# Kernel optimization log

Hardware: AMD Instinct MI355X
Metric: run time of the kernel (lower is better)

## Reference

```python
import jax, jax.numpy as jnp
import numpy as np

N_ROIS, ROI_DIM, D, H, L, FF, NCLS = 200, 199, 192, 6, 3, 576, 2
EPS = 1e-5

def _ln(x, g, b):
    m = jnp.mean(x, axis=-1, keepdims=True)
    v = jnp.mean((x - m) ** 2, axis=-1, keepdims=True)
    return (x - m) * jax.lax.rsqrt(v + EPS) * g + b

def _gelu(x):
    return jax.nn.gelu(x, approximate=False)

def _mha(q, k, v, Wqkv, bqkv, Wo, bo):
    # q: [B,Q,D], k/v: [B,S,D]; Wqkv: [3,D,D], bqkv: [3,D]
    B, Q, _ = q.shape
    S = k.shape[1]
    Dh = D // H
    qp = (q @ Wqkv[0] + bqkv[0]).reshape(B, Q, H, Dh)
    kp = (k @ Wqkv[1] + bqkv[1]).reshape(B, S, H, Dh)
    vp = (v @ Wqkv[2] + bqkv[2]).reshape(B, S, H, Dh)
    scores = jnp.einsum('bqhd,bkhd->bhqk', qp, kp) / jnp.sqrt(jnp.float32(Dh))
    attn = jax.nn.softmax(scores, axis=-1)
    out = jnp.einsum('bhqk,bkhd->bqhd', attn, vp).reshape(B, Q, D)
    return out @ Wo + bo

def setup_inputs() -> dict:
    key = jax.random.key(0)
    ks = iter(jax.random.split(key, 40))
    r = lambda *s: jax.random.normal(next(ks), s, dtype=jnp.float32) * 0.02
    inp = {
        'x': jax.random.normal(next(ks), (256, N_ROIS * ROI_DIM), dtype=jnp.float32),
        # 200 distinct per-ROI tokenizers, stacked for a single batched GEMM
        'roi_W': r(N_ROIS, ROI_DIM, D), 'roi_b': r(N_ROIS, D),
        'roi_ln_g': jnp.ones((N_ROIS, D), jnp.float32), 'roi_ln_b': jnp.zeros((N_ROIS, D), jnp.float32),
        'pos_emb': r(N_ROIS, D),
        # encoder layers stacked on leading L dim
        'enc_Wqkv': r(L, 3, D, D), 'enc_bqkv': r(L, 3, D),
        'enc_Wo': r(L, D, D), 'enc_bo': r(L, D),
        'enc_ln1_g': jnp.ones((L, D), jnp.float32), 'enc_ln1_b': jnp.zeros((L, D), jnp.float32),
        'enc_W1': r(L, D, FF), 'enc_b1': r(L, FF),
        'enc_W2': r(L, FF, D), 'enc_b2': r(L, D),
        'enc_ln2_g': jnp.ones((L, D), jnp.float32), 'enc_ln2_b': jnp.zeros((L, D), jnp.float32),
        # attention pooling MHA
        'pool_Wqkv': r(3, D, D), 'pool_bqkv': r(3, D),
        'pool_Wo': r(D, D), 'pool_bo': r(D),
        # classifier head
        'cls_ln_g': jnp.ones((D,), jnp.float32), 'cls_ln_b': jnp.zeros((D,), jnp.float32),
        'cls_W1': r(D, D // 2), 'cls_b1': r(D // 2),
        'cls_W2': r(D // 2, D // 4), 'cls_b2': r(D // 4),
        'cls_W3': r(D // 4, NCLS), 'cls_b3': r(NCLS),
    }
    return inp

def reference(x, roi_W, roi_b, roi_ln_g, roi_ln_b, pos_emb,
              enc_Wqkv, enc_bqkv, enc_Wo, enc_bo, enc_ln1_g, enc_ln1_b,
              enc_W1, enc_b1, enc_W2, enc_b2, enc_ln2_g, enc_ln2_b,
              pool_Wqkv, pool_bqkv, pool_Wo, pool_bo,
              cls_ln_g, cls_ln_b, cls_W1, cls_b1, cls_W2, cls_b2, cls_W3, cls_b3):
    B = x.shape[0]
    roi = x.reshape(B, N_ROIS, ROI_DIM)
    # fused per-ROI Linear (200 distinct weights) as one batched GEMM
    tok = jnp.einsum('brf,rfd->brd', roi, roi_W) + roi_b  # [B,200,192]
    tok = _gelu(_ln(tok, roi_ln_g, roi_ln_b))  # dropout = identity (eval)
    tok = tok + pos_emb[None]
    # post-norm transformer encoder (PyTorch default norm_first=False)
    h = tok
    for i in range(L):
        a = _mha(h, h, h, enc_Wqkv[i], enc_bqkv[i], enc_Wo[i], enc_bo[i])
        h = _ln(h + a, enc_ln1_g[i], enc_ln1_b[i])
        f = _gelu(h @ enc_W1[i] + enc_b1[i]) @ enc_W2[i] + enc_b2[i]
        h = _ln(h + f, enc_ln2_g[i], enc_ln2_b[i])
    # MHA pooling: query = mean over ROI tokens
    q = jnp.mean(h, axis=1, keepdims=True)  # [B,1,D]
    pooled = _mha(q, h, h, pool_Wqkv, pool_bqkv, pool_Wo, pool_bo)[:, 0]  # [B,D]
    # classifier
    z = _ln(pooled, cls_ln_g, cls_ln_b)
    z = _gelu(z @ cls_W1 + cls_b1)
    z = _gelu(z @ cls_W2 + cls_b2)
    return z @ cls_W3 + cls_b3
```

## Files before the change

kernel.cpp:

```cpp
#include <hip/hip_runtime.h>
#include <math.h>


typedef unsigned short u16;
typedef unsigned int u32;
typedef __attribute__((ext_vector_type(8))) __bf16 bf16x8;
typedef __attribute__((ext_vector_type(4))) float f32x4;

#define GLL16(gp, lp) __builtin_amdgcn_global_load_lds(                 \
    (const __attribute__((address_space(1))) void*)(gp),                \
    (__attribute__((address_space(3))) void*)(lp), 16, 0, 0)

#define FENCE_VM()   do { asm volatile("s_waitcnt vmcnt(0)" ::: "memory");  \
                          __builtin_amdgcn_sched_barrier(0); } while (0)
#define FENCE_LGKM() do { asm volatile("s_waitcnt lgkmcnt(0)" ::: "memory");\
                          __builtin_amdgcn_sched_barrier(0); } while (0)

__device__ __forceinline__ u16 f2bf(float x) {
    u32 u = __float_as_uint(x);
    u = (u + 0x7FFFu + ((u >> 16) & 1u)) >> 16;
    return (u16)u;
}
__device__ __forceinline__ float bf2f(u16 h) {
    return __uint_as_float(((u32)h) << 16);
}

__device__ __forceinline__ float gelu_exact(float x) {
    return 0.5f * x * (1.0f + erff(x * 0.7071067811865475f));
}

__device__ __forceinline__ float wave_sum(float v) {
#pragma unroll
    for (int o = 32; o > 0; o >>= 1) v += __shfl_xor(v, o, 64);
    return v;
}
__device__ __forceinline__ float wave_max(float v) {
#pragma unroll
    for (int o = 32; o > 0; o >>= 1) v = fmaxf(v, __shfl_xor(v, o, 64));
    return v;
}
__device__ __forceinline__ float row_sum16(float v) {
    v += __shfl_xor(v, 1, 64); v += __shfl_xor(v, 2, 64);
    v += __shfl_xor(v, 4, 64); v += __shfl_xor(v, 8, 64);
    return v;
}

__device__ __forceinline__ f32x4 mfma_bf16(bf16x8 a, bf16x8 b, f32x4 c) {
    return __builtin_amdgcn_mfma_f32_16x16x32_bf16(a, b, c, 0, 0, 0);
}

__global__ void conv_wt(const float* __restrict__ W, u16* __restrict__ oh,
                        int K, int N)
{
    const long z = blockIdx.z;
    const int idx = blockIdx.x * 256 + threadIdx.x;
    if (idx >= K * N) return;
    const int k = idx / N, n = idx - k * N;
    const float x = W[z * K * N + idx];
    oh[z * (long)K * N + (long)n * K + k] = f2bf(x);
}

__global__ void conv_x(const float* __restrict__ x, u16* __restrict__ xh)
{
    const long idx = (long)blockIdx.x * 256 + threadIdx.x;
    if (idx >= 200L * 256 * 224) return;
    const int k = (int)(idx % 224);
    const long t = idx / 224;
    const int m = (int)(t % 256);
    const int z = (int)(t / 256);
    const float v = (k < 199) ? x[(long)m * 39800 + z * 199 + k] : 0.f;
    xh[idx] = f2bf(v);
}

__global__ void conv_roiw(const float* __restrict__ W, u16* __restrict__ oh)
{
    __shared__ float tile[32][33];
    const int z = blockIdx.z;
    const int k0 = blockIdx.x * 32;
    const int n0 = blockIdx.y * 32;
    for (int i = threadIdx.y; i < 32; i += 8) {
        const int k = k0 + i, n = n0 + threadIdx.x;
        tile[i][threadIdx.x] = (k < 199) ? W[((long)z * 199 + k) * 192 + n] : 0.f;
    }
    __syncthreads();
    for (int i = threadIdx.y; i < 32; i += 8) {
        const int n = n0 + i, k = k0 + threadIdx.x;
        const float v = tile[threadIdx.x][i];
        oh[((long)z * 192 + n) * 224 + k] = f2bf(v);
    }
}

template<int EPI>
__global__ __launch_bounds__(256, 3) void gemm_ns(
    const u16* __restrict__ Ah,
    const u16* __restrict__ Bh,
    const float* __restrict__ bias,
    float* __restrict__ C, u16* __restrict__ Ch,
    int N, int K)
{
    __shared__ u16 Ash[128][32];
    __shared__ u16 Bsh[192][32];

    const int tid = threadIdx.x;
    const int wave = tid >> 6, lane = tid & 63;
    const int lm = lane & 15, quad = lane >> 4;
    const int wm = wave >> 1, wn = wave & 1;
    const long m0 = (long)blockIdx.x * 128;
    const int n0 = blockIdx.y * 192;
    const int lrow = lane >> 2;
    const int lch  = (((lane & 3) ^ (lrow & 3)) * 8);
    const int sq   = (quad ^ (lm & 3)) * 8;

    const u16* pA0h = Ah + (m0 + wave * 32 +  0 + lrow) * K + lch;
    const u16* pA1h = Ah + (m0 + wave * 32 + 16 + lrow) * K + lch;
    const u16* pB0h = Bh + (long)(n0 + wave * 48 +  0 + lrow) * K + lch;
    const u16* pB1h = Bh + (long)(n0 + wave * 48 + 16 + lrow) * K + lch;
    const u16* pB2h = Bh + (long)(n0 + wave * 48 + 32 + lrow) * K + lch;

    auto stage = [&](int k0) {
        GLL16(pA0h + k0, &Ash[wave * 32][0]);
        GLL16(pA1h + k0, &Ash[wave * 32 + 16][0]);
        GLL16(pB0h + k0, &Bsh[wave * 48][0]);
        GLL16(pB1h + k0, &Bsh[wave * 48 + 16][0]);
        GLL16(pB2h + k0, &Bsh[wave * 48 + 32][0]);
    };

    f32x4 acc[4][6];
#pragma unroll
    for (int i = 0; i < 4; i++)
#pragma unroll
        for (int j = 0; j < 6; j++)
#pragma unroll
            for (int r = 0; r < 4; r++) acc[i][j][r] = 0.f;

    const int kt = K >> 5;
    stage(0);
    FENCE_VM();
    __syncthreads();

    for (int t = 0; t < kt; t++) {
        bf16x8 afh[4];
#pragma unroll
        for (int mi = 0; mi < 4; mi++)
            afh[mi] = *(const bf16x8*)&Ash[wm * 64 + mi * 16 + lm][sq];
#pragma unroll
        for (int jh = 0; jh < 2; jh++) {
            bf16x8 bfh[3];
#pragma unroll
            for (int j = 0; j < 3; j++)
                bfh[j] = *(const bf16x8*)&Bsh[wn * 96 + (jh * 3 + j) * 16 + lm][sq];
#pragma unroll
            for (int mi = 0; mi < 4; mi++)
#pragma unroll
                for (int j = 0; j < 3; j++)
                    acc[mi][jh * 3 + j] =
                        mfma_bf16(afh[mi], bfh[j], acc[mi][jh * 3 + j]);
        }
        if (t + 1 < kt) {
            __syncthreads();
            stage((t + 1) << 5);
            FENCE_VM();
            __syncthreads();
        }
    }

#pragma unroll
    for (int mi = 0; mi < 4; mi++) {
        const long rowb = m0 + wm * 64 + mi * 16 + quad * 4;
#pragma unroll
        for (int nj = 0; nj < 6; nj++) {
            const int col = n0 + wn * 96 + nj * 16 + lm;
            const float bv = bias[col];
#pragma unroll
            for (int r = 0; r < 4; r++) {
                float v = acc[mi][nj][r] + bv;
                if (EPI == 0) {
                    C[(rowb + r) * N + col] = v;
                } else {
                    if (EPI == 2) v = gelu_exact(v);
                    Ch[(rowb + r) * N + col] = f2bf(v);
                }
            }
        }
    }
}

__global__ __launch_bounds__(256, 3) void gemm_ln(
    const u16* __restrict__ Ah,
    const u16* __restrict__ Bh,
    const float* __restrict__ bias,
    u16* __restrict__ Hh, u16* __restrict__ Hl,
    const float* __restrict__ lng, const float* __restrict__ lnb,
    int K)
{
    __shared__ u16 Ash[128][32];
    __shared__ u16 Bsh[192][32];

    const int tid = threadIdx.x;
    const int wave = tid >> 6, lane = tid & 63;
    const int lm = lane & 15, quad = lane >> 4;
    const long m0 = (long)blockIdx.x * 128;
    const int lrow = lane >> 2;
    const int lch  = (((lane & 3) ^ (lrow & 3)) * 8);
    const int sq   = (quad ^ (lm & 3)) * 8;

    const u16* pA0h = Ah + (m0 + wave * 32 +  0 + lrow) * K + lch;
    const u16* pA1h = Ah + (m0 + wave * 32 + 16 + lrow) * K + lch;
    const u16* pB0h = Bh + (long)(wave * 48 +  0 + lrow) * K + lch;
    const u16* pB1h = Bh + (long)(wave * 48 + 16 + lrow) * K + lch;
    const u16* pB2h = Bh + (long)(wave * 48 + 32 + lrow) * K + lch;

    auto stage = [&](int k0) {
        GLL16(pA0h + k0, &Ash[wave * 32][0]);
        GLL16(pA1h + k0, &Ash[wave * 32 + 16][0]);
        GLL16(pB0h + k0, &Bsh[wave * 48][0]);
        GLL16(pB1h + k0, &Bsh[wave * 48 + 16][0]);
        GLL16(pB2h + k0, &Bsh[wave * 48 + 32][0]);
    };

    f32x4 acc[2][12];
#pragma unroll
    for (int i = 0; i < 2; i++)
#pragma unroll
        for (int j = 0; j < 12; j++)
#pragma unroll
            for (int r = 0; r < 4; r++) acc[i][j][r] = 0.f;

    const int kt = K >> 5;
    stage(0);
    FENCE_VM();
    __syncthreads();

    for (int t = 0; t < kt; t++) {
        bf16x8 afh[2];
#pragma unroll
        for (int mi = 0; mi < 2; mi++)
            afh[mi] = *(const bf16x8*)&Ash[wave * 32 + mi * 16 + lm][sq];
#pragma unroll
        for (int g = 0; g < 4; g++) {
            bf16x8 bfh[3];
#pragma unroll
            for (int j = 0; j < 3; j++)
                bfh[j] = *(const bf16x8*)&Bsh[g * 48 + j * 16 + lm][sq];
#pragma unroll
            for (int mi = 0; mi < 2; mi++)
#pragma unroll
                for (int j = 0; j < 3; j++) {
                    const int ni = g * 3 + j;
                    acc[mi][ni] = mfma_bf16(afh[mi], bfh[j], acc[mi][ni]);
                }
        }
        if (t + 1 < kt) {
            __syncthreads();
            stage((t + 1) << 5);
            FENCE_VM();
            __syncthreads();
        }
    }

    float gv[12], bv2[12], biasv[12];
#pragma unroll
    for (int ni = 0; ni < 12; ni++) {
        const int col = ni * 16 + lm;
        gv[ni] = lng[col]; bv2[ni] = lnb[col]; biasv[ni] = bias[col];
    }
#pragma unroll
    for (int mi = 0; mi < 2; mi++) {
#pragma unroll
        for (int r = 0; r < 4; r++) {
            const long row = m0 + wave * 32 + mi * 16 + quad * 4 + r;
            const long rb = row * 192;
            float vals[12];
            float s = 0.f;
#pragma unroll
            for (int ni = 0; ni < 12; ni++) {
                const int col = ni * 16 + lm;
                const float hval = bf2f(Hh[rb + col]) + bf2f(Hl[rb + col]);
                vals[ni] = acc[mi][ni][r] + biasv[ni] + hval;
                s += vals[ni];
            }
            const float mean = row_sum16(s) * (1.f / 192.f);
            float ss = 0.f;
#pragma unroll
            for (int ni = 0; ni < 12; ni++) {
                vals[ni] -= mean;
                ss += vals[ni] * vals[ni];
            }
            const float var = row_sum16(ss) * (1.f / 192.f);
            const float rsr = 1.f / sqrtf(var + 1e-5f);
#pragma unroll
            for (int ni = 0; ni < 12; ni++) {
                const int col = ni * 16 + lm;
                const float y = vals[ni] * rsr * gv[ni] + bv2[ni];
                const u16 hb = f2bf(y);
                Hh[rb + col] = hb;
                Hl[rb + col] = f2bf(y - bf2f(hb));
            }
        }
    }
}

__global__ __launch_bounds__(256, 3) void tok_mfma(
    const u16* __restrict__ xh,
    const u16* __restrict__ wth,
    const float* __restrict__ roi_b,
    const float* __restrict__ lng, const float* __restrict__ lnb,
    const float* __restrict__ pos,
    u16* __restrict__ hh, u16* __restrict__ hl)
{
    __shared__ u16 Ash[128][32];
    __shared__ u16 Bsh[192][32];

    const int tid = threadIdx.x;
    const int wave = tid >> 6, lane = tid & 63;
    const int lm = lane & 15, quad = lane >> 4;
    const int m0 = blockIdx.x * 128;
    const int z = blockIdx.y;
    const int lrow = lane >> 2;
    const int lch  = (((lane & 3) ^ (lrow & 3)) * 8);
    const int sq   = (quad ^ (lm & 3)) * 8;
    const int K = 224;

    const u16* pA0h = xh + ((long)z * 256 + m0 + wave * 32 +  0 + lrow) * K + lch;
    const u16* pA1h = xh + ((long)z * 256 + m0 + wave * 32 + 16 + lrow) * K + lch;
    const u16* pB0h = wth + ((long)z * 192 + wave * 48 +  0 + lrow) * K + lch;
    const u16* pB1h = wth + ((long)z * 192 + wave * 48 + 16 + lrow) * K + lch;
    const u16* pB2h = wth + ((long)z * 192 + wave * 48 + 32 + lrow) * K + lch;

    auto stage = [&](int k0) {
        GLL16(pA0h + k0, &Ash[wave * 32][0]);
        GLL16(pA1h + k0, &Ash[wave * 32 + 16][0]);
        GLL16(pB0h + k0, &Bsh[wave * 48][0]);
        GLL16(pB1h + k0, &Bsh[wave * 48 + 16][0]);
        GLL16(pB2h + k0, &Bsh[wave * 48 + 32][0]);
    };

    f32x4 acc[2][12];
#pragma unroll
    for (int i = 0; i < 2; i++)
#pragma unroll
        for (int j = 0; j < 12; j++)
#pragma unroll
            for (int r = 0; r < 4; r++) acc[i][j][r] = 0.f;

    stage(0);
    FENCE_VM();
    __syncthreads();
    for (int t = 0; t < 7; t++) {
        bf16x8 afh[2];
#pragma unroll
        for (int mi = 0; mi < 2; mi++)
            afh[mi] = *(const bf16x8*)&Ash[wave * 32 + mi * 16 + lm][sq];
#pragma unroll
        for (int g = 0; g < 4; g++) {
            bf16x8 bfh[3];
#pragma unroll
            for (int j = 0; j < 3; j++)
                bfh[j] = *(const bf16x8*)&Bsh[g * 48 + j * 16 + lm][sq];
#pragma unroll
            for (int mi = 0; mi < 2; mi++)
#pragma unroll
                for (int j = 0; j < 3; j++) {
                    const int ni = g * 3 + j;
                    acc[mi][ni] = mfma_bf16(afh[mi], bfh[j], acc[mi][ni]);
                }
        }
        if (t + 1 < 7) {
            __syncthreads();
            stage((t + 1) << 5);
            FENCE_VM();
            __syncthreads();
        }
    }

    float gv[12], bv2[12], biasv[12], pv[12];
#pragma unroll
    for (int ni = 0; ni < 12; ni++) {
        const int col = ni * 16 + lm;
        gv[ni]    = lng[z * 192 + col];
        bv2[ni]   = lnb[z * 192 + col];
        biasv[ni] = roi_b[z * 192 + col];
        pv[ni]    = pos[z * 192 + col];
    }
#pragma unroll
    for (int mi = 0; mi < 2; mi++) {
#pragma unroll
        for (int r = 0; r < 4; r++) {
            const int brow = m0 + wave * 32 + mi * 16 + quad * 4 + r;
            float vals[12];
            float s = 0.f;
#pragma unroll
            for (int ni = 0; ni < 12; ni++) {
                vals[ni] = acc[mi][ni][r] + biasv[ni];
                s += vals[ni];
            }
            const float mean = row_sum16(s) * (1.f / 192.f);
            float ss = 0.f;
#pragma unroll
            for (int ni = 0; ni < 12; ni++) {
                vals[ni] -= mean;
                ss += vals[ni] * vals[ni];
            }
            const float var = row_sum16(ss) * (1.f / 192.f);
            const float rsr = 1.f / sqrtf(var + 1e-5f);
            const long ob = ((long)brow * 200 + z) * 192;
#pragma unroll
            for (int ni = 0; ni < 12; ni++) {
                const int col = ni * 16 + lm;
                const float y = gelu_exact(vals[ni] * rsr * gv[ni] + bv2[ni]) + pv[ni];
                const u16 hb = f2bf(y);
                hh[ob + col] = hb;
                hl[ob + col] = f2bf(y - bf2f(hb));
            }
        }
    }
}

template<int EPI>
__global__ __launch_bounds__(256) void gemm_kernel(
    const float* __restrict__ A, int lda, long strideA,
    const float* __restrict__ Bw, long strideB,
    const float* __restrict__ bias, long strideBias,
    float* __restrict__ C, int ldc, long strideC,
    int M, int N, int K, int ldb)
{
    __shared__ float As[16][132];
    __shared__ float Bs[16][68];

    const int z = blockIdx.z;
    const float* Ab    = A    + (long)z * strideA;
    const float* Bb    = Bw   + (long)z * strideB;
    const float* biasb = bias + (long)z * strideBias;
    float*       Cb    = C    + (long)z * strideC;

    const int row0 = blockIdx.x * 128;
    const int col0 = blockIdx.y * 64;
    const int tid  = threadIdx.x;
    const int tm = tid >> 4;
    const int tn = tid & 15;

    const int la_m = tid >> 1;
    const int la_k = (tid & 1) * 8;
    const int lb_k = tid >> 4;
    const int lb_n = (tid & 15) * 4;

    const float* bcol = Bb + (col0 + lb_n);
    const float* arow = Ab + (long)(row0 + la_m) * lda;
    const bool vecA = ((lda & 3) == 0) &&
                      ((((unsigned long long)(const void*)arow) & 15ull) == 0ull);

    float acc[8][4];
#pragma unroll
    for (int i = 0; i < 8; i++)
#pragma unroll
        for (int j = 0; j < 4; j++) acc[i][j] = 0.f;

    for (int k0 = 0; k0 < K; k0 += 16) {
        if (vecA && (k0 + 16 <= K)) {
            float4 v0 = *(const float4*)(arow + k0 + la_k);
            float4 v1 = *(const float4*)(arow + k0 + la_k + 4);
            As[la_k + 0][la_m] = v0.x; As[la_k + 1][la_m] = v0.y;
            As[la_k + 2][la_m] = v0.z; As[la_k + 3][la_m] = v0.w;
            As[la_k + 4][la_m] = v1.x; As[la_k + 5][la_m] = v1.y;
            As[la_k + 6][la_m] = v1.z; As[la_k + 7][la_m] = v1.w;
        } else {
#pragma unroll
            for (int i = 0; i < 8; i++) {
                int k = k0 + la_k + i;
                As[la_k + i][la_m] = (k < K) ? arow[k] : 0.f;
            }
        }
        {
            int k = k0 + lb_k;
            float4 v = make_float4(0.f, 0.f, 0.f, 0.f);
            if (k < K) v = *(const float4*)(bcol + (long)k * ldb);
            *(float4*)&Bs[lb_k][lb_n] = v;
        }
        __syncthreads();
#pragma unroll
        for (int kk = 0; kk < 16; kk++) {
            float4 a0 = *(const float4*)&As[kk][tm * 8];
            float4 a1 = *(const float4*)&As[kk][tm * 8 + 4];
            float4 b4 = *(const float4*)&Bs[kk][tn * 4];
            float av[8] = {a0.x, a0.y, a0.z, a0.w, a1.x, a1.y, a1.z, a1.w};
            float bv[4] = {b4.x, b4.y, b4.z, b4.w};
#pragma unroll
            for (int i = 0; i < 8; i++)
#pragma unroll
                for (int j = 0; j < 4; j++) acc[i][j] += av[i] * bv[j];
        }
        __syncthreads();
    }

    const int gcol = col0 + tn * 4;
    float4 bv4 = *(const float4*)(biasb + gcol);
#pragma unroll
    for (int i = 0; i < 8; i++) {
        int grow = row0 + tm * 8 + i;
        float4 o;
        o.x = acc[i][0] + bv4.x; o.y = acc[i][1] + bv4.y;
        o.z = acc[i][2] + bv4.z; o.w = acc[i][3] + bv4.w;
        if (EPI == 1) {
            o.x = gelu_exact(o.x); o.y = gelu_exact(o.y);
            o.z = gelu_exact(o.z); o.w = gelu_exact(o.w);
        }
        *(float4*)(Cb + (long)grow * ldc + gcol) = o;
    }
}

__global__ __launch_bounds__(256, 2) void attn_enc_mfma(
    const u16* __restrict__ qkvh, u16* __restrict__ outh)
{
    __shared__ u16 Ksh[208][40];
    __shared__ u16 Vth[32][224];
    __shared__ u16 Pbuf[4][2][16][40];

    const int bh = blockIdx.x;
    const int b = bh / 6, h = bh % 6;
    const int tid = threadIdx.x;
    const int wave = tid >> 6, lane = tid & 63;
    const int lm = lane & 15, quad = lane >> 4;
    const int nq = (wave == 0) ? 4 : 3;

    uint4 qh[4];
#pragma unroll
    for (int i = 0; i < 4; i++) {
        if (i < nq) {
            int qt = wave + 4 * i;
            int qrow = qt * 16 + lm; if (qrow > 199) qrow = 199;
            const long off = (long)(b * 200 + qrow) * 576 + h * 32 + quad * 8;
            qh[i] = *(const uint4*)(qkvh + off);
        }
    }

    if (wave < 2) {
        const int sub = wave * 64 + lane;
#pragma unroll
        for (int rep = 0; rep < 7; rep++) {
            const int idx = rep * 128 + sub;
            if (idx < 208 * 4) {
                const int key = idx >> 2, ch = idx & 3;
                const bool valid = key < 200;
                const long roff = (long)(b * 200 + (valid ? key : 0)) * 576
                                  + h * 32 + 192 + ch * 8;
                uint4 v = valid ? *(const uint4*)(qkvh + roff)
                                : make_uint4(0, 0, 0, 0);
                *(uint4*)(&Ksh[0][0] + key * 40 + ch * 8) = v;
            }
        }
    } else {
        const int sub = (wave - 2) * 64 + lane;
#pragma unroll
        for (int rep = 0; rep < 4; rep++) {
            const int idx = rep * 128 + sub;
            if (idx < 224 * 2) {
                const int key = idx >> 1, hf = idx & 1;
                const bool valid = key < 200;
                const long roff = (long)(b * 200 + (valid ? key : 0)) * 576
                                  + h * 32 + 384 + hf * 16;
                uint4 v0 = valid ? *(const uint4*)(qkvh + roff)
                                 : make_uint4(0, 0, 0, 0);
                uint4 v1 = valid ? *(const uint4*)(qkvh + roff + 8)
                                 : make_uint4(0, 0, 0, 0);
                const u16* p0 = (const u16*)&v0;
                const u16* p1 = (const u16*)&v1;
#pragma unroll
                for (int j = 0; j < 8; j++) {
                    Vth[hf * 16 + j][key]     = p0[j];
                    Vth[hf * 16 + 8 + j][key] = p1[j];
                }
            }
        }
    }
    __syncthreads();

    const float scale = 0.17677669529663688f;
    int par = 0;
    float lrow[4][4];
    f32x4 accO[4][2];

#pragma unroll
    for (int i = 0; i < 4; i++) {
        if (i >= nq) continue;
        const bf16x8 qhf = *(const bf16x8*)&qh[i];
        float s[13][4];
#pragma unroll
        for (int ni = 0; ni < 13; ni++) {
            bf16x8 kh8 = *(const bf16x8*)&Ksh[ni * 16 + lm][quad * 8];
            f32x4 c = {0.f, 0.f, 0.f, 0.f};
            c = mfma_bf16(qhf, kh8, c);
            const bool masked = (ni * 16 + lm) >= 200;
#pragma unroll
            for (int r = 0; r < 4; r++)
                s[ni][r] = masked ? -1e30f : c[r] * scale;
        }
#pragma unroll
        for (int r = 0; r < 4; r++) {
            float pm = s[0][r];
#pragma unroll
            for (int ni = 1; ni < 13; ni++) pm = fmaxf(pm, s[ni][r]);
            pm = fmaxf(pm, __shfl_xor(pm, 1, 64));
            pm = fmaxf(pm, __shfl_xor(pm, 2, 64));
            pm = fmaxf(pm, __shfl_xor(pm, 4, 64));
            pm = fmaxf(pm, __shfl_xor(pm, 8, 64));
            float ps = 0.f;
#pragma unroll
            for (int ni = 0; ni < 13; ni++) {
                float e = __expf(s[ni][r] - pm);
                s[ni][r] = e;
                ps += e;
            }
            ps += __shfl_xor(ps, 1, 64);
            ps += __shfl_xor(ps, 2, 64);
            ps += __shfl_xor(ps, 4, 64);
            ps += __shfl_xor(ps, 8, 64);
            lrow[i][r] = ps;
            accO[i][0][r] = 0.f;
            accO[i][1][r] = 0.f;
        }
#pragma unroll
        for (int ck = 0; ck < 7; ck++) {
            const int pb = par & 1; par++;
#pragma unroll
            for (int tl = 0; tl < 2; tl++) {
                const int t = 2 * ck + tl;
#pragma unroll
                for (int r = 0; r < 4; r++) {
                    const float val = (t < 13) ? s[t][r] : 0.f;
                    Pbuf[wave][pb][quad * 4 + r][tl * 16 + lm] = f2bf(val);
                }
            }
            FENCE_LGKM();
            const bf16x8 pa = *(const bf16x8*)&Pbuf[wave][pb][lm][quad * 8];
#pragma unroll
            for (int nt = 0; nt < 2; nt++) {
                bf16x8 vh8 = *(const bf16x8*)&Vth[nt * 16 + lm][ck * 32 + quad * 8];
                accO[i][nt] = mfma_bf16(pa, vh8, accO[i][nt]);
            }
        }
    }

#pragma unroll
    for (int i = 0; i < 4; i++) {
        if (i >= nq) continue;
        const int qt = wave + 4 * i;
#pragma unroll
        for (int r = 0; r < 4; r++) {
            const int qrow = qt * 16 + quad * 4 + r;
            if (qrow >= 200) continue;
            const float inv = 1.f / lrow[i][r];
            const long ob = (long)(b * 200 + qrow) * 192 + h * 32 + lm;
            outh[ob]      = f2bf(accO[i][0][r] * inv);
            outh[ob + 16] = f2bf(accO[i][1][r] * inv);
        }
    }
}

__global__ __launch_bounds__(192) void mean_tokens_pair(
    const u16* __restrict__ hh, const u16* __restrict__ hl, float* __restrict__ qmean)
{
    const int b = blockIdx.x, d = threadIdx.x;
    float s = 0.f;
    for (int r = 0; r < 200; r++) {
        const long idx = ((long)b * 200 + r) * 192 + d;
        s += bf2f(hh[idx]) + bf2f(hl[idx]);
    }
    qmean[b * 192 + d] = s * (1.f / 200.f);
}

__global__ __launch_bounds__(64) void attn_pool(
    const float* __restrict__ qp, const float* __restrict__ kv,
    float* __restrict__ out)
{
    __shared__ float p[200];
    const int b = blockIdx.x / 6, h = blockIdx.x % 6;
    const int lane = threadIdx.x;

    const float* qrow = qp + b * 192 + h * 32;
    float qr[32];
#pragma unroll
    for (int u = 0; u < 8; u++) {
        float4 t = *(const float4*)(qrow + 4 * u);
        qr[4 * u] = t.x; qr[4 * u + 1] = t.y;
        qr[4 * u + 2] = t.z; qr[4 * u + 3] = t.w;
    }
    const float scale = 0.17677669529663688f;
    const float* kb = kv + (long)(b * 200) * 384 + h * 32;
    float s[4];
    float mymax = -1e30f;
#pragma unroll
    for (int g = 0; g < 4; g++) {
        int j = lane + 64 * g;
        if (j < 200) {
            const float* kr = kb + (long)j * 384;
            float acc = 0.f;
#pragma unroll
            for (int u = 0; u < 8; u++) {
                float4 k4 = *(const float4*)(kr + 4 * u);
                acc += qr[4 * u] * k4.x + qr[4 * u + 1] * k4.y +
                       qr[4 * u + 2] * k4.z + qr[4 * u + 3] * k4.w;
            }
            s[g] = acc * scale;
            mymax = fmaxf(mymax, s[g]);
        } else {
            s[g] = -1e30f;
        }
    }
    float mx = wave_max(mymax);
    float psum = 0.f;
#pragma unroll
    for (int g = 0; g < 4; g++) {
        int j = lane + 64 * g;
        if (j < 200) {
            float e = __expf(s[g] - mx);
            p[j] = e;
            psum += e;
        }
    }
    float tot = wave_sum(psum);
    __syncthreads();
    const int half = lane >> 5, d = lane & 31;
    const float* vb = kv + (long)(b * 200) * 384 + 192 + h * 32 + d;
    float acc = 0.f;
    for (int jj = 0; jj < 100; jj++) {
        int j = half * 100 + jj;
        acc += p[j] * vb[(long)j * 384];
    }
    acc += __shfl_xor(acc, 32, 64);
    acc /= tot;
    if (lane < 32) out[b * 192 + h * 32 + d] = acc;
}

__global__ __launch_bounds__(64) void classifier_kernel(
    const float* __restrict__ pooled,
    const float* __restrict__ g, const float* __restrict__ bt,
    const float* __restrict__ W1, const float* __restrict__ b1,
    const float* __restrict__ W2, const float* __restrict__ b2,
    const float* __restrict__ W3, const float* __restrict__ b3,
    float* __restrict__ out)
{
    __shared__ float z[192];
    __shared__ float z1[96];
    __shared__ float z2[48];
    const int b = blockIdx.x, lane = threadIdx.x;
    const float* pr = pooled + b * 192;
    float x0 = pr[lane], x1 = pr[lane + 64], x2 = pr[lane + 128];
    float m = wave_sum(x0 + x1 + x2) * (1.f / 192.f);
    float d0 = x0 - m, d1 = x1 - m, d2 = x2 - m;
    float v = wave_sum(d0 * d0 + d1 * d1 + d2 * d2) * (1.f / 192.f);
    float rs = 1.f / sqrtf(v + 1e-5f);
    z[lane]       = d0 * rs * g[lane]       + bt[lane];
    z[lane + 64]  = d1 * rs * g[lane + 64]  + bt[lane + 64];
    z[lane + 128] = d2 * rs * g[lane + 128] + bt[lane + 128];
    __syncthreads();
#pragma unroll
    for (int rep = 0; rep < 2; rep++) {
        int j = lane + rep * 64;
        if (j < 96) {
            float a = b1[j];
            for (int k = 0; k < 192; k++) a += z[k] * W1[k * 96 + j];
            z1[j] = gelu_exact(a);
        }
    }
    __syncthreads();
    if (lane < 48) {
        float a = b2[lane];
        for (int k = 0; k < 96; k++) a += z1[k] * W2[k * 48 + lane];
        z2[lane] = gelu_exact(a);
    }
    __syncthreads();
    if (lane < 2) {
        float a = b3[lane];
        for (int k = 0; k < 48; k++) a += z2[k] * W3[k * 2 + lane];
        out[b * 2 + lane] = a;
    }
}

extern "C" void kernel_launch(void* const* d_in, const int* in_sizes, int n_in,
                              void* d_out, int out_size, void* d_ws, size_t ws_size,
                              hipStream_t stream)
{
    (void)in_sizes; (void)n_in; (void)out_size; (void)ws_size;

    const float* x         = (const float*)d_in[0];
    const float* roi_W     = (const float*)d_in[1];
    const float* roi_b     = (const float*)d_in[2];
    const float* roi_ln_g  = (const float*)d_in[3];
    const float* roi_ln_b  = (const float*)d_in[4];
    const float* pos_emb   = (const float*)d_in[5];
    const float* enc_Wqkv  = (const float*)d_in[6];
    const float* enc_bqkv  = (const float*)d_in[7];
    const float* enc_Wo    = (const float*)d_in[8];
    const float* enc_bo    = (const float*)d_in[9];
    const float* enc_ln1_g = (const float*)d_in[10];
    const float* enc_ln1_b = (const float*)d_in[11];
    const float* enc_W1    = (const float*)d_in[12];
    const float* enc_b1    = (const float*)d_in[13];
    const float* enc_W2    = (const float*)d_in[14];
    const float* enc_b2    = (const float*)d_in[15];
    const float* enc_ln2_g = (const float*)d_in[16];
    const float* enc_ln2_b = (const float*)d_in[17];
    const float* pool_Wqkv = (const float*)d_in[18];
    const float* pool_bqkv = (const float*)d_in[19];
    const float* pool_Wo   = (const float*)d_in[20];
    const float* pool_bo   = (const float*)d_in[21];
    const float* cls_ln_g  = (const float*)d_in[22];
    const float* cls_ln_b  = (const float*)d_in[23];
    const float* cls_W1    = (const float*)d_in[24];
    const float* cls_b1    = (const float*)d_in[25];
    const float* cls_W2    = (const float*)d_in[26];
    const float* cls_b2    = (const float*)d_in[27];
    const float* cls_W3    = (const float*)d_in[28];
    const float* cls_b3    = (const float*)d_in[29];

    char* ws = (char*)d_ws;
    u16*   hh    = (u16*)(ws);
    u16*   hl    = (u16*)(ws + 19660800);
    char*  bufA  = ws + 39321600;
    float* bufAf = (float*)bufA;
    u16*   xh    = (u16*)bufA;
    u16*   wth   = (u16*)(bufA + 45875200);
    u16*   qkvh  = (u16*)bufA;
    u16*   ffh   = (u16*)bufA;
    char*  bufB  = ws + 157286400;
    u16*   bBh   = (u16*)bufB;
    float* qmean = (float*)(ws + 196608000);
    float* qp    = qmean + 49152;
    float* pattn = qp + 49152;
    float* pooled= pattn + 49152;
    char*  wts   = ws + 197394432;
    u16* WqkvH = (u16*)(wts);
    u16* Wff1H = (u16*)(wts + 1327104);
    u16* Wff2H = (u16*)(wts + 2654208);
    u16* WwoH  = (u16*)(wts + 3981312);
    u16* WkvH  = (u16*)(wts + 4423680);

    conv_wt<<<dim3(144, 1, 9), 256, 0, stream>>>(enc_Wqkv, WqkvH, 192, 192);
    conv_wt<<<dim3(432, 1, 3), 256, 0, stream>>>(enc_W1, Wff1H, 192, 576);
    conv_wt<<<dim3(432, 1, 3), 256, 0, stream>>>(enc_W2, Wff2H, 576, 192);
    conv_wt<<<dim3(144, 1, 3), 256, 0, stream>>>(enc_Wo, WwoH, 192, 192);
    conv_wt<<<dim3(144, 1, 2), 256, 0, stream>>>(pool_Wqkv + 36864, WkvH, 192, 192);

    conv_x<<<44800, 256, 0, stream>>>(x, xh);
    conv_roiw<<<dim3(7, 6, 200), dim3(32, 8), 0, stream>>>(roi_W, wth);
    tok_mfma<<<dim3(2, 200), 256, 0, stream>>>(
        xh, wth, roi_b, roi_ln_g, roi_ln_b, pos_emb, hh, hl);

    for (int i = 0; i < 3; i++) {
        gemm_ns<3><<<dim3(400, 3), 256, 0, stream>>>(
            hh, WqkvH + (long)i * 110592,
            enc_bqkv + i * 576, nullptr, qkvh, 576, 192);
        attn_enc_mfma<<<1536, 256, 0, stream>>>(qkvh, bBh);
        gemm_ln<<<dim3(400, 1), 256, 0, stream>>>(
            bBh, WwoH + (long)i * 36864,
            enc_bo + i * 192,
            hh, hl, enc_ln1_g + i * 192, enc_ln1_b + i * 192, 192);
        gemm_ns<2><<<dim3(400, 3), 256, 0, stream>>>(
            hh, Wff1H + (long)i * 110592,
            enc_b1 + i * 576, nullptr, ffh, 576, 192);
        gemm_ln<<<dim3(400, 1), 256, 0, stream>>>(
            ffh, Wff2H + (long)i * 110592,
            enc_b2 + i * 192,
            hh, hl, enc_ln2_g + i * 192, enc_ln2_b + i * 192, 576);
    }

    mean_tokens_pair<<<256, 192, 0, stream>>>(hh, hl, qmean);
    gemm_kernel<0><<<dim3(2, 3, 1), 256, 0, stream>>>(
        qmean, 192, 0, pool_Wqkv, 0, pool_bqkv, 0, qp, 192, 0, 256, 192, 192, 192);
    gemm_ns<0><<<dim3(400, 2), 256, 0, stream>>>(
        hh, WkvH, pool_bqkv + 192, bufAf, nullptr, 384, 192);
    attn_pool<<<1536, 64, 0, stream>>>(qp, bufAf, pattn);
    gemm_kernel<0><<<dim3(2, 3, 1), 256, 0, stream>>>(
        pattn, 192, 0, pool_Wo, 0, pool_bo, 0, pooled, 192, 0, 256, 192, 192, 192);

    classifier_kernel<<<256, 64, 0, stream>>>(
        pooled, cls_ln_g, cls_ln_b,
        cls_W1, cls_b1, cls_W2, cls_b2, cls_W3, cls_b3,
        (float*)d_out);
}
```

Baseline: 873.1 us.

## Merge weight conversion launches, batch P-tile stores, and use bf16 pooled K/V

The five weight transpose/convert launches become one kernel that picks its source and destination from blockIdx.z. In encoder attention, the P tiles for two key chunks are written before a single LDS wait, instead of one wait per chunk. The pooling K/V projection now writes bf16 through gemm_ns<3> instead of fp32, and attn_pool reads bf16, halving that traffic. The cost is lower K/V precision in pooling, plus many idle blocks in the merged conversion grid, since every z slice gets 432 blocks.

```diff
diff --git a/kernel.cpp b/kernel.cpp
--- a/kernel.cpp
+++ b/kernel.cpp
@@ -49,15 +49,25 @@
     return __builtin_amdgcn_mfma_f32_16x16x32_bf16(a, b, c, 0, 0, 0);
 }
 
-__global__ void conv_wt(const float* __restrict__ W, u16* __restrict__ oh,
-                        int K, int N)
-{
-    const long z = blockIdx.z;
+__global__ void conv_wt_all(
+    const float* __restrict__ Wqkv, const float* __restrict__ W1,
+    const float* __restrict__ W2,   const float* __restrict__ Wo,
+    const float* __restrict__ Wkv,
+    u16* __restrict__ oqkv, u16* __restrict__ o1, u16* __restrict__ o2,
+    u16* __restrict__ oo,   u16* __restrict__ okv)
+{
+    const int z = blockIdx.z;
+    const float* W; u16* o; int K, N, s;
+    if (z < 9)       { W = Wqkv; o = oqkv; K = 192; N = 192; s = z; }
+    else if (z < 12) { W = W1;   o = o1;   K = 192; N = 576; s = z - 9; }
+    else if (z < 15) { W = W2;   o = o2;   K = 576; N = 192; s = z - 12; }
+    else if (z < 18) { W = Wo;   o = oo;   K = 192; N = 192; s = z - 15; }
+    else             { W = Wkv;  o = okv;  K = 192; N = 192; s = z - 18; }
     const int idx = blockIdx.x * 256 + threadIdx.x;
     if (idx >= K * N) return;
     const int k = idx / N, n = idx - k * N;
-    const float x = W[z * K * N + idx];
-    oh[z * (long)K * N + (long)n * K + k] = f2bf(x);
+    const float x = W[(long)s * K * N + idx];
+    o[(long)s * K * N + (long)n * K + k] = f2bf(x);
 }
 
 __global__ void conv_x(const float* __restrict__ x, u16* __restrict__ xh)
@@ -575,7 +585,6 @@
     __syncthreads();
 
     const float scale = 0.17677669529663688f;
-    int par = 0;
     float lrow[4][4];
     f32x4 accO[4][2];
 
@@ -619,23 +628,32 @@
             accO[i][1][r] = 0.f;
         }
 #pragma unroll
-        for (int ck = 0; ck < 7; ck++) {
-            const int pb = par & 1; par++;
-#pragma unroll
-            for (int tl = 0; tl < 2; tl++) {
-                const int t = 2 * ck + tl;
-#pragma unroll
-                for (int r = 0; r < 4; r++) {
-                    const float val = (t < 13) ? s[t][r] : 0.f;
-                    Pbuf[wave][pb][quad * 4 + r][tl * 16 + lm] = f2bf(val);
+        for (int cp = 0; cp < 4; cp++) {
+#pragma unroll
+            for (int half = 0; half < 2; half++) {
+                const int ck = 2 * cp + half;
+                if (ck >= 7) continue;
+#pragma unroll
+                for (int tl = 0; tl < 2; tl++) {
+                    const int t = 2 * ck + tl;
+#pragma unroll
+                    for (int r = 0; r < 4; r++) {
+                        const float val = (t < 13) ? s[t][r] : 0.f;
+                        Pbuf[wave][half][quad * 4 + r][tl * 16 + lm] = f2bf(val);
+                    }
                 }
             }
             FENCE_LGKM();
-            const bf16x8 pa = *(const bf16x8*)&Pbuf[wave][pb][lm][quad * 8];
-#pragma unroll
-            for (int nt = 0; nt < 2; nt++) {
-                bf16x8 vh8 = *(const bf16x8*)&Vth[nt * 16 + lm][ck * 32 + quad * 8];
-                accO[i][nt] = mfma_bf16(pa, vh8, accO[i][nt]);
+#pragma unroll
+            for (int half = 0; half < 2; half++) {
+                const int ck = 2 * cp + half;
+                if (ck >= 7) continue;
+                const bf16x8 pa = *(const bf16x8*)&Pbuf[wave][half][lm][quad * 8];
+#pragma unroll
+                for (int nt = 0; nt < 2; nt++) {
+                    bf16x8 vh8 = *(const bf16x8*)&Vth[nt * 16 + lm][ck * 32 + quad * 8];
+                    accO[i][nt] = mfma_bf16(pa, vh8, accO[i][nt]);
+                }
             }
         }
     }
@@ -669,7 +687,7 @@
 }
 
 __global__ __launch_bounds__(64) void attn_pool(
-    const float* __restrict__ qp, const float* __restrict__ kv,
+    const float* __restrict__ qp, const u16* __restrict__ kv,
     float* __restrict__ out)
 {
     __shared__ float p[200];
@@ -685,20 +703,22 @@
         qr[4 * u + 2] = t.z; qr[4 * u + 3] = t.w;
     }
     const float scale = 0.17677669529663688f;
-    const float* kb = kv + (long)(b * 200) * 384 + h * 32;
+    const u16* kb = kv + (long)(b * 200) * 384 + h * 32;
     float s[4];
     float mymax = -1e30f;
 #pragma unroll
     for (int g = 0; g < 4; g++) {
         int j = lane + 64 * g;
         if (j < 200) {
-            const float* kr = kb + (long)j * 384;
+            const u16* kr = kb + (long)j * 384;
             float acc = 0.f;
 #pragma unroll
-            for (int u = 0; u < 8; u++) {
-                float4 k4 = *(const float4*)(kr + 4 * u);
-                acc += qr[4 * u] * k4.x + qr[4 * u + 1] * k4.y +
-                       qr[4 * u + 2] * k4.z + qr[4 * u + 3] * k4.w;
+            for (int u = 0; u < 4; u++) {
+                uint4 k8 = *(const uint4*)(kr + 8 * u);
+                const u16* kp = (const u16*)&k8;
+#pragma unroll
+                for (int j2 = 0; j2 < 8; j2++)
+                    acc += qr[8 * u + j2] * bf2f(kp[j2]);
             }
             s[g] = acc * scale;
             mymax = fmaxf(mymax, s[g]);
@@ -720,11 +740,11 @@
     float tot = wave_sum(psum);
     __syncthreads();
     const int half = lane >> 5, d = lane & 31;
-    const float* vb = kv + (long)(b * 200) * 384 + 192 + h * 32 + d;
+    const u16* vb = kv + (long)(b * 200) * 384 + 192 + h * 32 + d;
     float acc = 0.f;
     for (int jj = 0; jj < 100; jj++) {
         int j = half * 100 + jj;
-        acc += p[j] * vb[(long)j * 384];
+        acc += p[j] * bf2f(vb[(long)j * 384]);
     }
     acc += __shfl_xor(acc, 32, 64);
     acc /= tot;
@@ -817,11 +837,11 @@
     u16*   hh    = (u16*)(ws);
     u16*   hl    = (u16*)(ws + 19660800);
     char*  bufA  = ws + 39321600;
-    float* bufAf = (float*)bufA;
     u16*   xh    = (u16*)bufA;
     u16*   wth   = (u16*)(bufA + 45875200);
     u16*   qkvh  = (u16*)bufA;
     u16*   ffh   = (u16*)bufA;
+    u16*   kvb   = (u16*)bufA;
     char*  bufB  = ws + 157286400;
     u16*   bBh   = (u16*)bufB;
     float* qmean = (float*)(ws + 196608000);
@@ -835,11 +855,9 @@
     u16* WwoH  = (u16*)(wts + 3981312);
     u16* WkvH  = (u16*)(wts + 4423680);
 
-    conv_wt<<<dim3(144, 1, 9), 256, 0, stream>>>(enc_Wqkv, WqkvH, 192, 192);
-    conv_wt<<<dim3(432, 1, 3), 256, 0, stream>>>(enc_W1, Wff1H, 192, 576);
-    conv_wt<<<dim3(432, 1, 3), 256, 0, stream>>>(enc_W2, Wff2H, 576, 192);
-    conv_wt<<<dim3(144, 1, 3), 256, 0, stream>>>(enc_Wo, WwoH, 192, 192);
-    conv_wt<<<dim3(144, 1, 2), 256, 0, stream>>>(pool_Wqkv + 36864, WkvH, 192, 192);
+    conv_wt_all<<<dim3(432, 1, 20), 256, 0, stream>>>(
+        enc_Wqkv, enc_W1, enc_W2, enc_Wo, pool_Wqkv + 36864,
+        WqkvH, Wff1H, Wff2H, WwoH, WkvH);
 
     conv_x<<<44800, 256, 0, stream>>>(x, xh);
     conv_roiw<<<dim3(7, 6, 200), dim3(32, 8), 0, stream>>>(roi_W, wth);
@@ -867,9 +885,9 @@
     mean_tokens_pair<<<256, 192, 0, stream>>>(hh, hl, qmean);
     gemm_kernel<0><<<dim3(2, 3, 1), 256, 0, stream>>>(
         qmean, 192, 0, pool_Wqkv, 0, pool_bqkv, 0, qp, 192, 0, 256, 192, 192, 192);
-    gemm_ns<0><<<dim3(400, 2), 256, 0, stream>>>(
-        hh, WkvH, pool_bqkv + 192, bufAf, nullptr, 384, 192);
-    attn_pool<<<1536, 64, 0, stream>>>(qp, bufAf, pattn);
+    gemm_ns<3><<<dim3(400, 2), 256, 0, stream>>>(
+        hh, WkvH, pool_bqkv + 192, nullptr, kvb, 384, 192);
+    attn_pool<<<1536, 64, 0, stream>>>(qp, kvb, pattn);
     gemm_kernel<0><<<dim3(2, 3, 1), 256, 0, stream>>>(
         pattn, 192, 0, pool_Wo, 0, pool_bo, 0, pooled, 192, 0, 256, 192, 192, 192);
 
```

Measured after the change: 1.171 ms. +34.1%, slower.
